# Performance work log

Measured on AMD Instinct MI355X. Metric: run time of the kernel, lower is better.

## Reference

```python
import jax, jax.numpy as jnp
import numpy as np

N = 50000      # nodes
E = 800000     # edges (undirected, stored once)
D_IN = 128
D_OUT = 128


def setup_inputs() -> dict:
    key = jax.random.key(0)
    k1, k2, k3, k4 = jax.random.split(key, 4)
    X = jax.random.normal(k1, (N, D_IN), dtype=jnp.float32)
    edges = jax.random.randint(k2, (E, 2), 0, N, dtype=jnp.int32)
    weights = jax.random.uniform(k3, (E,), dtype=jnp.float32)
    # glorot_uniform kernel W: [D_IN, D_OUT]
    limit = np.sqrt(6.0 / (D_IN + D_OUT)).astype(np.float32)
    W = jax.random.uniform(k4, (D_IN, D_OUT), dtype=jnp.float32, minval=-limit, maxval=limit)
    return {"X": X, "edges": edges, "weights": weights, "W": W}


def reference(X, edges, weights, W):
    # D^{-1} @ A @ X @ W with A the symmetric weighted adjacency from the edge list.
    # nx.Graph is undirected -> each edge contributes in both directions.
    src = jnp.concatenate([edges[:, 0], edges[:, 1]])   # [2E]
    dst = jnp.concatenate([edges[:, 1], edges[:, 0]])   # [2E]
    w = jnp.concatenate([weights, weights])             # [2E]
    # (A @ X)[i] = sum over edges (j -> i) of w * X[j]
    ax = jax.ops.segment_sum(w[:, None] * X[src], dst, num_segments=N)  # [N, D_IN]
    deg = jax.ops.segment_sum(w, dst, num_segments=N)                   # [N]
    inv_deg = jnp.where(deg > 0, 1.0 / deg, 0.0)                        # D^{-1} (safe for isolated nodes)
    return (ax * inv_deg[:, None]) @ W                                  # [N, D_OUT]
```

## Files before the change

### kernel.cpp

```cpp
#include <hip/hip_runtime.h>
#include <hip/hip_fp16.h>

#define NN 50000
#define NE 800000
#define D  128
#define NB 391
#define NS 256
#define EPS 3125
#define SN (NB * NS)
#define SCB 1024
#define NSB ((SN + SCB - 1) / SCB)

#define OFF_SLAB 0
#define OFF_XW   0
#define OFF_CSR4 12800000
#define OFF_HIST 19200000
#define OFF_BASE 19600384
#define OFF_BSUM 20000768
#define OFF_ROW  20001280
#define OFF_WF   20201344
#define NEED_A   20234112

#define OFF_CNT  0
#define OFF_ROWF 200704
#define OFF_CUR  401408
#define OFF_CSR8 602112

typedef float v2f  __attribute__((ext_vector_type(2)));
typedef __attribute__((ext_vector_type(8))) short bf16x8;
typedef __attribute__((ext_vector_type(4))) float f32x4;

__device__ __forceinline__ float bf_lo(unsigned int v) { return __uint_as_float(v << 16); }
__device__ __forceinline__ float bf_hi(unsigned int v) { return __uint_as_float(v & 0xffff0000u); }
__device__ __forceinline__ float wdec(unsigned int v) {
    return __half2float(__ushort_as_half((unsigned short)(v >> 16)));
}
__device__ __forceinline__ unsigned short bf16rne(float f) {
    unsigned int b = __float_as_uint(f);
    return (unsigned short)((b + 0x7fffu + ((b >> 16) & 1u)) >> 16);
}

__global__ __launch_bounds__(256) void gc_shist(
    const int2* __restrict__ edges, int* __restrict__ histT)
{
    __shared__ int h[NB];
    const int s = blockIdx.x;
    for (int i = threadIdx.x; i < NB; i += 256) h[i] = 0;
    __syncthreads();
    const int e0 = s * EPS;
    for (int i = threadIdx.x; i < EPS; i += 256) {
        int2 p = edges[e0 + i];
        atomicAdd(&h[p.y >> 7], 1);
        atomicAdd(&h[p.x >> 7], 1);
    }
    __syncthreads();
    for (int b = threadIdx.x; b < NB; b += 256) histT[b * NS + s] = h[b];
}

__global__ __launch_bounds__(256) void gc_scanA(
    const int* __restrict__ in, int* __restrict__ bsum)
{
    __shared__ int red[256];
    int base = blockIdx.x * SCB;
    int s = 0;
    for (int i = threadIdx.x; i < SCB; i += 256) {
        int idx = base + i;
        s += (idx < SN) ? in[idx] : 0;
    }
    red[threadIdx.x] = s;
    __syncthreads();
    for (int off = 128; off > 0; off >>= 1) {
        if (threadIdx.x < off) red[threadIdx.x] += red[threadIdx.x + off];
        __syncthreads();
    }
    if (threadIdx.x == 0) bsum[blockIdx.x] = red[0];
}

__global__ __launch_bounds__(1024) void gc_scanB(int* __restrict__ bsum)
{
    __shared__ int part[1024];
    int t = threadIdx.x;
    int v = (t < NSB) ? bsum[t] : 0;
    part[t] = v;
    __syncthreads();
    for (int off = 1; off < 1024; off <<= 1) {
        int x = (t >= off) ? part[t - off] : 0;
        __syncthreads();
        part[t] += x;
        __syncthreads();
    }
    if (t < NSB) bsum[t] = part[t] - v;
}

__global__ __launch_bounds__(256) void gc_scanC(
    const int* __restrict__ in, const int* __restrict__ bsum,
    int* __restrict__ baseT)
{
    __shared__ int part[256];
    int base = blockIdx.x * SCB;
    int idx0 = base + threadIdx.x * 4;
    int4 v = make_int4(0, 0, 0, 0);
    if (idx0 + 3 < SN) v = *reinterpret_cast<const int4*>(in + idx0);
    int s = v.x + v.y + v.z + v.w;
    part[threadIdx.x] = s;
    __syncthreads();
    for (int off = 1; off < 256; off <<= 1) {
        int x = (threadIdx.x >= off) ? part[threadIdx.x - off] : 0;
        __syncthreads();
        part[threadIdx.x] += x;
        __syncthreads();
    }
    int run = bsum[blockIdx.x] + part[threadIdx.x] - s;
    if (idx0 + 3 < SN)
        *reinterpret_cast<int4*>(baseT + idx0) =
            make_int4(run, run + v.x, run + v.x + v.y, run + v.x + v.y + v.z);
}

__global__ __launch_bounds__(256) void gc_sscat(
    const int2* __restrict__ edges, const float* __restrict__ wts,
    const int* __restrict__ baseT, int2* __restrict__ slab)
{
    __shared__ int cur[NB];
    const int s = blockIdx.x;
    for (int b = threadIdx.x; b < NB; b += 256) cur[b] = baseT[b * NS + s];
    __syncthreads();
    const int e0 = s * EPS;
    for (int i = threadIdx.x; i < EPS; i += 256) {
        int2 p = edges[e0 + i];
        int wb = __float_as_int(wts[e0 + i]);
        int b = p.y >> 7;
        int pos = atomicAdd(&cur[b], 1);
        slab[pos] = make_int2(p.x | ((p.y & 127) << 16), wb);
        b = p.x >> 7;
        pos = atomicAdd(&cur[b], 1);
        slab[pos] = make_int2(p.y | ((p.x & 127) << 16), wb);
    }
}

__global__ __launch_bounds__(256) void gc_csr(
    const int* __restrict__ baseT, const int2* __restrict__ slab,
    int* __restrict__ row_start, unsigned int* __restrict__ csr4)
{
    __shared__ int ncnt[128], ncur[128], part[128];
    const int tid = threadIdx.x;
    const int b = blockIdx.x;
    const int start = baseT[b * NS];
    const int end = (b == NB - 1) ? (2 * NE) : baseT[(b + 1) * NS];

    if (tid < 128) ncnt[tid] = 0;
    __syncthreads();

    for (int j = start + tid; j < end; j += 256)
        atomicAdd(&ncnt[(slab[j].x >> 16) & 127], 1);
    __syncthreads();

    if (tid < 128) part[tid] = ncnt[tid];
    __syncthreads();
    for (int off = 1; off < 128; off <<= 1) {
        int v = 0;
        if (tid < 128 && tid >= off) v = part[tid - off];
        __syncthreads();
        if (tid < 128) part[tid] += v;
        __syncthreads();
    }
    if (tid < 128) {
        int st = start + part[tid] - ncnt[tid];
        int n = b * 128 + tid;
        if (n < NN) row_start[n] = st;
        ncur[tid] = st;
    }
    if (b == 0 && tid == 0) row_start[NN] = 2 * NE;
    __syncthreads();

    for (int j = start + tid; j < end; j += 256) {
        int2 en = slab[j];
        int dl = (en.x >> 16) & 127;
        unsigned int hb =
            (unsigned int)__half_as_ushort(__float2half_rn(__int_as_float(en.y))) << 16;
        int pos = atomicAdd(&ncur[dl], 1);
        csr4[pos] = (unsigned int)(en.x & 0xffff) | hb;
    }
}

__global__ __launch_bounds__(256) void gc_wfrag(
    const float* __restrict__ Wm, unsigned short* __restrict__ wf)
{
    int t = blockIdx.x * 256 + threadIdx.x;
    int j    = t & 7;
    int lane = (t >> 3) & 63;
    int nt   = (t >> 9) & 7;
    int ki   = t >> 12;
    int k = ki * 32 + (lane >> 4) * 8 + j;
    int n = nt * 16 + (lane & 15);
    wf[t] = bf16rne(Wm[k * D + n]);
}

__global__ __launch_bounds__(256) void gc_gemm_mfma(
    const float* __restrict__ X, const unsigned short* __restrict__ wf,
    unsigned short* __restrict__ dst)
{
    const int lane = threadIdx.x & 63;
    const int wave = threadIdx.x >> 6;
    const int rbase = blockIdx.x * 64 + wave * 16;
    const int r  = lane & 15;
    const int kb = lane >> 4;

    f32x4 acc[8];
    #pragma unroll
    for (int i = 0; i < 8; ++i) acc[i] = f32x4{0.f, 0.f, 0.f, 0.f};

    const bf16x8* wfv = reinterpret_cast<const bf16x8*>(wf);
    const int row = rbase + r;
    const bool rok = row < NN;

    #pragma unroll
    for (int ki = 0; ki < 4; ++ki) {
        float4 a0 = make_float4(0.f, 0.f, 0.f, 0.f);
        float4 a1 = make_float4(0.f, 0.f, 0.f, 0.f);
        if (rok) {
            const float4* xp = reinterpret_cast<const float4*>(
                X + (size_t)row * D + ki * 32 + kb * 8);
            a0 = xp[0];
            a1 = xp[1];
        }
        bf16x8 af;
        af[0] = (short)bf16rne(a0.x); af[1] = (short)bf16rne(a0.y);
        af[2] = (short)bf16rne(a0.z); af[3] = (short)bf16rne(a0.w);
        af[4] = (short)bf16rne(a1.x); af[5] = (short)bf16rne(a1.y);
        af[6] = (short)bf16rne(a1.z); af[7] = (short)bf16rne(a1.w);
        #pragma unroll
        for (int nt = 0; nt < 8; ++nt) {
            bf16x8 bf = wfv[(ki * 8 + nt) * 64 + lane];
            acc[nt] = __builtin_amdgcn_mfma_f32_16x16x32_bf16(af, bf, acc[nt], 0, 0, 0);
        }
    }

    const int orow0 = rbase + kb * 4;
    #pragma unroll
    for (int nt = 0; nt < 8; ++nt) {
        #pragma unroll
        for (int reg = 0; reg < 4; ++reg) {
            int orow = orow0 + reg;
            if (orow < NN)
                dst[(size_t)orow * D + nt * 16 + r] = bf16rne(acc[nt][reg]);
        }
    }
}

__global__ __launch_bounds__(256) void gc_gather4(
    const int* __restrict__ row_start, const unsigned int* __restrict__ csr4,
    const unsigned int* __restrict__ F, float* __restrict__ out)
{
    int wid  = (blockIdx.x * 256 + threadIdx.x) >> 6;
    unsigned int lane = threadIdx.x & 63;
    if (wid >= NN) return;
    int j   = row_start[wid];
    int end = row_start[wid + 1];
    v2f acc = {0.f, 0.f};
    float dw = 0.f;
    for (; j + 8 <= end; j += 8) {
        unsigned int e0 = csr4[j],     e1 = csr4[j + 1];
        unsigned int e2 = csr4[j + 2], e3 = csr4[j + 3];
        unsigned int e4 = csr4[j + 4], e5 = csr4[j + 5];
        unsigned int e6 = csr4[j + 6], e7 = csr4[j + 7];
        unsigned int v0 = F[((e0 & 0xffffu) << 6) | lane];
        unsigned int v1 = F[((e1 & 0xffffu) << 6) | lane];
        unsigned int v2 = F[((e2 & 0xffffu) << 6) | lane];
        unsigned int v3 = F[((e3 & 0xffffu) << 6) | lane];
        unsigned int v4 = F[((e4 & 0xffffu) << 6) | lane];
        unsigned int v5 = F[((e5 & 0xffffu) << 6) | lane];
        unsigned int v6 = F[((e6 & 0xffffu) << 6) | lane];
        unsigned int v7 = F[((e7 & 0xffffu) << 6) | lane];
        float w0 = wdec(e0), w1 = wdec(e1), w2 = wdec(e2), w3 = wdec(e3);
        float w4 = wdec(e4), w5 = wdec(e5), w6 = wdec(e6), w7 = wdec(e7);
        acc += w0 * v2f{bf_lo(v0), bf_hi(v0)};
        acc += w1 * v2f{bf_lo(v1), bf_hi(v1)};
        acc += w2 * v2f{bf_lo(v2), bf_hi(v2)};
        acc += w3 * v2f{bf_lo(v3), bf_hi(v3)};
        acc += w4 * v2f{bf_lo(v4), bf_hi(v4)};
        acc += w5 * v2f{bf_lo(v5), bf_hi(v5)};
        acc += w6 * v2f{bf_lo(v6), bf_hi(v6)};
        acc += w7 * v2f{bf_lo(v7), bf_hi(v7)};
        dw += (w0 + w1 + w2 + w3) + (w4 + w5 + w6 + w7);
    }
    for (; j < end; ++j) {
        unsigned int e0 = csr4[j];
        unsigned int v0 = F[((e0 & 0xffffu) << 6) | lane];
        float w0 = wdec(e0);
        acc += w0 * v2f{bf_lo(v0), bf_hi(v0)};
        dw += w0;
    }
    float inv = dw > 0.f ? 1.f / dw : 0.f;
    float2 r; r.x = acc.x * inv; r.y = acc.y * inv;
    reinterpret_cast<float2*>(out)[(size_t)wid * 64 + lane] = r;
}

__global__ __launch_bounds__(256) void gc_hist(
    const int2* __restrict__ edges, int* __restrict__ counts)
{
    int e = blockIdx.x * 256 + threadIdx.x;
    if (e >= NE) return;
    int2 p = edges[e];
    atomicAdd(counts + p.x, 1);
    atomicAdd(counts + p.y, 1);
}

__global__ __launch_bounds__(1024) void gc_scan(
    const int* __restrict__ counts, int* __restrict__ row_start,
    int* __restrict__ cursor)
{
    const int CHUNK = (NN + 1023) / 1024;
    __shared__ int part[1024];
    int t = threadIdx.x;
    int lo = t * CHUNK, hi = min(lo + CHUNK, NN);
    int s = 0;
    for (int i = lo; i < hi; ++i) s += counts[i];
    part[t] = s;
    __syncthreads();
    for (int off = 1; off < 1024; off <<= 1) {
        int v = (t >= off) ? part[t - off] : 0;
        __syncthreads();
        part[t] += v;
        __syncthreads();
    }
    int run = part[t] - s;
    for (int i = lo; i < hi; ++i) {
        int c = counts[i];
        row_start[i] = run;
        cursor[i]    = run;
        run += c;
    }
    if (t == 1023) row_start[NN] = part[1023];
}

__global__ __launch_bounds__(256) void gc_fill8(
    const int2* __restrict__ edges, const float* __restrict__ wts,
    int* __restrict__ cursor, int2* __restrict__ csr)
{
    int e = blockIdx.x * 256 + threadIdx.x;
    if (e >= NE) return;
    int2 p = edges[e];
    int wb = __float_as_int(wts[e]);
    int pos = atomicAdd(cursor + p.y, 1);
    csr[pos] = make_int2(p.x, wb);
    pos = atomicAdd(cursor + p.x, 1);
    csr[pos] = make_int2(p.y, wb);
}

__global__ __launch_bounds__(256) void gc_gather_f32(
    const int* __restrict__ row_start, const int2* __restrict__ csr,
    const float* __restrict__ F, float* __restrict__ out)
{
    int wid  = (blockIdx.x * 256 + threadIdx.x) >> 6;
    int lane = threadIdx.x & 63;
    if (wid >= NN) return;
    int j   = row_start[wid];
    int end = row_start[wid + 1];
    const float2* F2 = reinterpret_cast<const float2*>(F);
    float ax = 0.f, ay = 0.f, dw = 0.f;
    for (; j < end; ++j) {
        int2  cw = csr[j];
        float w  = __int_as_float(cw.y);
        float2 xv = F2[(size_t)cw.x * 64 + lane];
        ax = fmaf(w, xv.x, ax);
        ay = fmaf(w, xv.y, ay);
        dw += w;
    }
    float inv = dw > 0.f ? 1.f / dw : 0.f;
    float2 r; r.x = ax * inv; r.y = ay * inv;
    reinterpret_cast<float2*>(out)[(size_t)wid * 64 + lane] = r;
}

__global__ __launch_bounds__(256) void gc_gemm_f32(
    const float* __restrict__ src, float* __restrict__ dst,
    const float* __restrict__ Wm)
{
    __shared__ float Ws[D * D];
    __shared__ float axs[16 * D];
    const int tid = threadIdx.x;
    const int col = tid & 127;
    const int ty  = tid >> 7;
    const int rbase = blockIdx.x * 16;

    const float4* W4  = reinterpret_cast<const float4*>(Wm);
    float4*       Ws4 = reinterpret_cast<float4*>(Ws);
    #pragma unroll
    for (int i = 0; i < 16; ++i) Ws4[tid + i * 256] = W4[tid + i * 256];

    const float4* A4   = reinterpret_cast<const float4*>(src + (size_t)rbase * D);
    float4*       axs4 = reinterpret_cast<float4*>(axs);
    #pragma unroll
    for (int i = 0; i < 2; ++i) axs4[tid + i * 256] = A4[tid + i * 256];
    __syncthreads();

    float acc[8];
    #pragma unroll
    for (int i = 0; i < 8; ++i) acc[i] = 0.f;

    for (int k = 0; k < D; ++k) {
        float wv = Ws[k * D + col];
        #pragma unroll
        for (int i = 0; i < 8; ++i)
            acc[i] = fmaf(axs[(ty * 8 + i) * D + k], wv, acc[i]);
    }

    #pragma unroll
    for (int i = 0; i < 8; ++i)
        dst[(size_t)(rbase + ty * 8 + i) * D + col] = acc[i];
}

extern "C" void kernel_launch(void* const* d_in, const int* in_sizes, int n_in,
                              void* d_out, int out_size, void* d_ws, size_t ws_size,
                              hipStream_t stream) {
    const float* X     = (const float*)d_in[0];
    const int2*  edges = (const int2*)d_in[1];
    const float* wts   = (const float*)d_in[2];
    const float* Wm    = (const float*)d_in[3];
    float* out = (float*)d_out;
    char*  ws  = (char*)d_ws;

    const int eblocks = (NE + 255) / 256;

    if (ws_size >= NEED_A) {
        int2* slab  = (int2*)(ws + OFF_SLAB);
        unsigned int* csr4 = (unsigned int*)(ws + OFF_CSR4);
        int*  histT = (int*)(ws + OFF_HIST);
        int*  baseT = (int*)(ws + OFF_BASE);
        int*  bsum  = (int*)(ws + OFF_BSUM);
        int*  row   = (int*)(ws + OFF_ROW);
        unsigned short* wf = (unsigned short*)(ws + OFF_WF);
        unsigned short* xw = (unsigned short*)(ws + OFF_XW);

        gc_shist<<<NS, 256, 0, stream>>>(edges, histT);
        gc_scanA<<<NSB, 256, 0, stream>>>(histT, bsum);
        gc_scanB<<<1, 1024, 0, stream>>>(bsum);
        gc_scanC<<<NSB, 256, 0, stream>>>(histT, bsum, baseT);
        gc_sscat<<<NS, 256, 0, stream>>>(edges, wts, baseT, slab);
        gc_wfrag<<<64, 256, 0, stream>>>(Wm, wf);
        gc_csr<<<NB, 256, 0, stream>>>(baseT, slab, row, csr4);
        gc_gemm_mfma<<<(NN + 63) / 64, 256, 0, stream>>>(X, wf, xw);
        gc_gather4<<<(NN * 64 + 255) / 256, 256, 0, stream>>>(
            row, csr4, (const unsigned int*)xw, out);
    } else {
        int*  counts    = (int*) (ws + OFF_CNT);
        int*  row_start = (int*) (ws + OFF_ROWF);
        int*  cursor    = (int*) (ws + OFF_CUR);
        int2* csr       = (int2*)(ws + OFF_CSR8);

        hipMemsetAsync(counts, 0, NN * sizeof(int), stream);
        gc_hist<<<eblocks, 256, 0, stream>>>(edges, counts);
        gc_scan<<<1, 1024, 0, stream>>>(counts, row_start, cursor);
        gc_fill8<<<eblocks, 256, 0, stream>>>(edges, wts, cursor, csr);
        gc_gather_f32<<<(NN * 64 + 255) / 256, 256, 0, stream>>>(row_start, csr, X, out);
        gc_gemm_f32<<<NN / 16, 256, 0, stream>>>(out, out, Wm);
    }
}
```

Before: 114.3 us.

## Stage scatter and CSR build in LDS for coalesced global writes

The bucket scatter kernel now counts and locally sorts each slice's edges into shared memory, then writes the sorted bucket runs to the global slab contiguously using a binary search over local bucket offsets. The CSR build kernel similarly sorts each block's entries into an LDS buffer and copies it out coalesced, falling back to direct global scatter when a block exceeds the LDS capacity. This targets the scattered, uncoalesced global writes of the two preprocessing kernels. In exchange it adds an extra edge read pass, a binary search per element, and large LDS use (about 50KB in the scatter kernel), which lowers occupancy.

```diff
diff --git a/kernel.cpp b/kernel.cpp
--- a/kernel.cpp
+++ b/kernel.cpp
@@ -7,9 +7,11 @@
 #define NB 391
 #define NS 256
 #define EPS 3125
+#define EPB (2 * EPS)
 #define SN (NB * NS)
 #define SCB 1024
 #define NSB ((SN + SCB - 1) / SCB)
+#define LCAP 5632
 
 #define OFF_SLAB 0
 #define OFF_XW   0
@@ -116,36 +118,78 @@
             make_int4(run, run + v.x, run + v.x + v.y, run + v.x + v.y + v.z);
 }
 
-__global__ __launch_bounds__(256) void gc_sscat(
+__global__ __launch_bounds__(256) void gc_sscat2(
     const int2* __restrict__ edges, const float* __restrict__ wts,
     const int* __restrict__ baseT, int2* __restrict__ slab)
 {
-    __shared__ int cur[NB];
-    const int s = blockIdx.x;
-    for (int b = threadIdx.x; b < NB; b += 256) cur[b] = baseT[b * NS + s];
-    __syncthreads();
-    const int e0 = s * EPS;
-    for (int i = threadIdx.x; i < EPS; i += 256) {
+    __shared__ int2 ebuf[EPB];
+    __shared__ int  sc[512];
+    __shared__ int  lbE[NB + 1];
+    __shared__ int  cur[NB];
+    __shared__ int  gb[NB];
+
+    const int s   = blockIdx.x;
+    const int tid = threadIdx.x;
+    const int e0  = s * EPS;
+
+    sc[tid] = 0; sc[tid + 256] = 0;
+    __syncthreads();
+
+    for (int i = tid; i < EPS; i += 256) {
+        int2 p = edges[e0 + i];
+        atomicAdd(&sc[p.y >> 7], 1);
+        atomicAdd(&sc[p.x >> 7], 1);
+    }
+    for (int b = tid; b < NB; b += 256) gb[b] = baseT[b * NS + s];
+    __syncthreads();
+
+    int own0 = sc[tid], own1 = sc[tid + 256];
+    for (int off = 1; off < 512; off <<= 1) {
+        int v0 = (tid >= off) ? sc[tid - off] : 0;
+        int v1 = (tid + 256 >= off) ? sc[tid + 256 - off] : 0;
+        __syncthreads();
+        sc[tid] += v0; sc[tid + 256] += v1;
+        __syncthreads();
+    }
+    if (tid < NB)       { lbE[tid] = sc[tid] - own0;       cur[tid] = lbE[tid]; }
+    int t1 = tid + 256;
+    if (t1 < NB)        { lbE[t1]  = sc[t1] - own1;        cur[t1]  = lbE[t1]; }
+    if (tid == 0) lbE[NB] = EPB;
+    __syncthreads();
+
+    for (int i = tid; i < EPS; i += 256) {
         int2 p = edges[e0 + i];
         int wb = __float_as_int(wts[e0 + i]);
         int b = p.y >> 7;
         int pos = atomicAdd(&cur[b], 1);
-        slab[pos] = make_int2(p.x | ((p.y & 127) << 16), wb);
+        ebuf[pos] = make_int2(p.x | ((p.y & 127) << 16), wb);
         b = p.x >> 7;
         pos = atomicAdd(&cur[b], 1);
-        slab[pos] = make_int2(p.y | ((p.x & 127) << 16), wb);
-    }
-}
-
-__global__ __launch_bounds__(256) void gc_csr(
+        ebuf[pos] = make_int2(p.y | ((p.x & 127) << 16), wb);
+    }
+    __syncthreads();
+
+    for (int idx = tid; idx < EPB; idx += 256) {
+        int lo = 0, hi = NB - 1;
+        while (lo < hi) {
+            int mid = (lo + hi + 1) >> 1;
+            if (lbE[mid] <= idx) lo = mid; else hi = mid - 1;
+        }
+        slab[gb[lo] + (idx - lbE[lo])] = ebuf[idx];
+    }
+}
+
+__global__ __launch_bounds__(256) void gc_csr2(
     const int* __restrict__ baseT, const int2* __restrict__ slab,
     int* __restrict__ row_start, unsigned int* __restrict__ csr4)
 {
     __shared__ int ncnt[128], ncur[128], part[128];
+    __shared__ unsigned int cbuf[LCAP];
     const int tid = threadIdx.x;
     const int b = blockIdx.x;
     const int start = baseT[b * NS];
     const int end = (b == NB - 1) ? (2 * NE) : baseT[(b + 1) * NS];
+    const int sz = end - start;
 
     if (tid < 128) ncnt[tid] = 0;
     __syncthreads();
@@ -164,21 +208,35 @@
         __syncthreads();
     }
     if (tid < 128) {
-        int st = start + part[tid] - ncnt[tid];
+        int stl = part[tid] - ncnt[tid];
         int n = b * 128 + tid;
-        if (n < NN) row_start[n] = st;
-        ncur[tid] = st;
+        if (n < NN) row_start[n] = start + stl;
+        ncur[tid] = stl;
     }
     if (b == 0 && tid == 0) row_start[NN] = 2 * NE;
     __syncthreads();
 
-    for (int j = start + tid; j < end; j += 256) {
-        int2 en = slab[j];
-        int dl = (en.x >> 16) & 127;
-        unsigned int hb =
-            (unsigned int)__half_as_ushort(__float2half_rn(__int_as_float(en.y))) << 16;
-        int pos = atomicAdd(&ncur[dl], 1);
-        csr4[pos] = (unsigned int)(en.x & 0xffff) | hb;
+    if (sz <= LCAP) {
+        for (int j = start + tid; j < end; j += 256) {
+            int2 en = slab[j];
+            int dl = (en.x >> 16) & 127;
+            unsigned int hb =
+                (unsigned int)__half_as_ushort(__float2half_rn(__int_as_float(en.y))) << 16;
+            int pos = atomicAdd(&ncur[dl], 1);
+            cbuf[pos] = (unsigned int)(en.x & 0xffff) | hb;
+        }
+        __syncthreads();
+        for (int idx = tid; idx < sz; idx += 256)
+            csr4[start + idx] = cbuf[idx];
+    } else {
+        for (int j = start + tid; j < end; j += 256) {
+            int2 en = slab[j];
+            int dl = (en.x >> 16) & 127;
+            unsigned int hb =
+                (unsigned int)__half_as_ushort(__float2half_rn(__int_as_float(en.y))) << 16;
+            int pos = atomicAdd(&ncur[dl], 1);
+            csr4[start + pos] = (unsigned int)(en.x & 0xffff) | hb;
+        }
     }
 }
 
@@ -435,9 +493,9 @@
         gc_scanA<<<NSB, 256, 0, stream>>>(histT, bsum);
         gc_scanB<<<1, 1024, 0, stream>>>(bsum);
         gc_scanC<<<NSB, 256, 0, stream>>>(histT, bsum, baseT);
-        gc_sscat<<<NS, 256, 0, stream>>>(edges, wts, baseT, slab);
+        gc_sscat2<<<NS, 256, 0, stream>>>(edges, wts, baseT, slab);
         gc_wfrag<<<64, 256, 0, stream>>>(Wm, wf);
-        gc_csr<<<NB, 256, 0, stream>>>(baseT, slab, row, csr4);
+        gc_csr2<<<NB, 256, 0, stream>>>(baseT, slab, row, csr4);
         gc_gemm_mfma<<<(NN + 63) / 64, 256, 0, stream>>>(X, wf, xw);
         gc_gather4<<<(NN * 64 + 255) / 256, 256, 0, stream>>>(
             row, csr4, (const unsigned int*)xw, out);
```

New measurement: 129.2 us. +13.0%, slower.

## Store XW in column-slab layout and gather in four column passes

Applied to the files above, without the earlier changes.

The GEMM now writes XW as four column slabs of 32 bf16 columns each, so one node's slab row is 64 bytes. The gather runs four passes, one per slab, with 16 lanes per node instead of a full wavefront. Each pass's random accesses then hit a 3.2 MB slab that fits better in cache, and more nodes are processed per wave. In exchange, every CSR entry is read four times, the per-node unroll drops to 4, and each node's output row is written in 64-byte pieces.

```diff
diff --git a/kernel.cpp b/kernel.cpp
--- a/kernel.cpp
+++ b/kernel.cpp
@@ -10,6 +10,8 @@
 #define SN (NB * NS)
 #define SCB 1024
 #define NSB ((SN + SCB - 1) / SCB)
+#define NPASS 4
+#define GPB 3125
 
 #define OFF_SLAB 0
 #define OFF_XW   0
@@ -238,61 +240,55 @@
     const int orow0 = rbase + kb * 4;
     #pragma unroll
     for (int nt = 0; nt < 8; ++nt) {
+        const int col = nt * 16 + r;
+        const size_t cbase = (size_t)(col >> 5) * (NN * 32) + (col & 31);
         #pragma unroll
         for (int reg = 0; reg < 4; ++reg) {
             int orow = orow0 + reg;
             if (orow < NN)
-                dst[(size_t)orow * D + nt * 16 + r] = bf16rne(acc[nt][reg]);
+                dst[cbase + (size_t)orow * 32] = bf16rne(acc[nt][reg]);
         }
     }
 }
 
-__global__ __launch_bounds__(256) void gc_gather4(
+__global__ __launch_bounds__(256) void gc_gather_p(
     const int* __restrict__ row_start, const unsigned int* __restrict__ csr4,
-    const unsigned int* __restrict__ F, float* __restrict__ out)
-{
-    int wid  = (blockIdx.x * 256 + threadIdx.x) >> 6;
-    unsigned int lane = threadIdx.x & 63;
-    if (wid >= NN) return;
-    int j   = row_start[wid];
-    int end = row_start[wid + 1];
+    const unsigned int* __restrict__ XWc, float* __restrict__ out)
+{
+    const int g  = blockIdx.x / GPB;
+    const int nb = blockIdx.x - g * GPB;
+    const int node = (nb * 256 + threadIdx.x) >> 4;
+    const unsigned int c = threadIdx.x & 15;
+    const unsigned int* F = XWc + (size_t)g * (NN * 16) + c;
+
+    int j   = row_start[node];
+    int end = row_start[node + 1];
     v2f acc = {0.f, 0.f};
     float dw = 0.f;
-    for (; j + 8 <= end; j += 8) {
+    for (; j + 4 <= end; j += 4) {
         unsigned int e0 = csr4[j],     e1 = csr4[j + 1];
         unsigned int e2 = csr4[j + 2], e3 = csr4[j + 3];
-        unsigned int e4 = csr4[j + 4], e5 = csr4[j + 5];
-        unsigned int e6 = csr4[j + 6], e7 = csr4[j + 7];
-        unsigned int v0 = F[((e0 & 0xffffu) << 6) | lane];
-        unsigned int v1 = F[((e1 & 0xffffu) << 6) | lane];
-        unsigned int v2 = F[((e2 & 0xffffu) << 6) | lane];
-        unsigned int v3 = F[((e3 & 0xffffu) << 6) | lane];
-        unsigned int v4 = F[((e4 & 0xffffu) << 6) | lane];
-        unsigned int v5 = F[((e5 & 0xffffu) << 6) | lane];
-        unsigned int v6 = F[((e6 & 0xffffu) << 6) | lane];
-        unsigned int v7 = F[((e7 & 0xffffu) << 6) | lane];
+        unsigned int v0 = F[(e0 & 0xffffu) << 4];
+        unsigned int v1 = F[(e1 & 0xffffu) << 4];
+        unsigned int v2 = F[(e2 & 0xffffu) << 4];
+        unsigned int v3 = F[(e3 & 0xffffu) << 4];
         float w0 = wdec(e0), w1 = wdec(e1), w2 = wdec(e2), w3 = wdec(e3);
-        float w4 = wdec(e4), w5 = wdec(e5), w6 = wdec(e6), w7 = wdec(e7);
         acc += w0 * v2f{bf_lo(v0), bf_hi(v0)};
         acc += w1 * v2f{bf_lo(v1), bf_hi(v1)};
         acc += w2 * v2f{bf_lo(v2), bf_hi(v2)};
         acc += w3 * v2f{bf_lo(v3), bf_hi(v3)};
-        acc += w4 * v2f{bf_lo(v4), bf_hi(v4)};
-        acc += w5 * v2f{bf_lo(v5), bf_hi(v5)};
-        acc += w6 * v2f{bf_lo(v6), bf_hi(v6)};
-        acc += w7 * v2f{bf_lo(v7), bf_hi(v7)};
-        dw += (w0 + w1 + w2 + w3) + (w4 + w5 + w6 + w7);
+        dw += (w0 + w1) + (w2 + w3);
     }
     for (; j < end; ++j) {
         unsigned int e0 = csr4[j];
-        unsigned int v0 = F[((e0 & 0xffffu) << 6) | lane];
+        unsigned int v0 = F[(e0 & 0xffffu) << 4];
         float w0 = wdec(e0);
         acc += w0 * v2f{bf_lo(v0), bf_hi(v0)};
         dw += w0;
     }
     float inv = dw > 0.f ? 1.f / dw : 0.f;
     float2 r; r.x = acc.x * inv; r.y = acc.y * inv;
-    reinterpret_cast<float2*>(out)[(size_t)wid * 64 + lane] = r;
+    reinterpret_cast<float2*>(out)[(size_t)node * 64 + g * 16 + c] = r;
 }
 
 __global__ __launch_bounds__(256) void gc_hist(
@@ -439,7 +435,7 @@
         gc_wfrag<<<64, 256, 0, stream>>>(Wm, wf);
         gc_csr<<<NB, 256, 0, stream>>>(baseT, slab, row, csr4);
         gc_gemm_mfma<<<(NN + 63) / 64, 256, 0, stream>>>(X, wf, xw);
-        gc_gather4<<<(NN * 64 + 255) / 256, 256, 0, stream>>>(
+        gc_gather_p<<<NPASS * GPB, 256, 0, stream>>>(
             row, csr4, (const unsigned int*)xw, out);
     } else {
         int*  counts    = (int*) (ws + OFF_CNT);
```

After: 124.8 us. 9.2% more time.
